# Performance work log

Hardware: AMD Instinct MI355X
Metric: run time of the kernel (lower is better)

Reference implementation:

```python
import jax, jax.numpy as jnp
import numpy as np

NUM_LAYERS = 2
HIDDEN = 512
INPUT = 512


def _lstm_cell(x, h, c, Wih, Whh, bih, bbh):
    # PyTorch LSTMCell: gates ordered i, f, g, o
    g = x @ Wih.T + bih + h @ Whh.T + bbh  # [B, 4H]
    i, f, gg, o = jnp.split(g, 4, axis=-1)
    c_new = jax.nn.sigmoid(f) * c + jax.nn.sigmoid(i) * jnp.tanh(gg)
    h_new = jax.nn.sigmoid(o) * jnp.tanh(c_new)
    return h_new, c_new


def setup_inputs() -> dict:
    key = jax.random.key(0)
    ks = jax.random.split(key, 8)
    B, T = 64, 512
    s = 1.0 / np.sqrt(HIDDEN)
    return {
        "x": jax.random.normal(ks[0], (B, T, INPUT), dtype=jnp.float32),
        "h0": jax.random.normal(ks[1], (NUM_LAYERS, B, HIDDEN), dtype=jnp.float32),
        "c0": jax.random.normal(ks[2], (NUM_LAYERS, B, HIDDEN), dtype=jnp.float32),
        # stacked per-layer weights (input_size == hidden_size so shapes match)
        "W_ih": jax.random.uniform(ks[3], (NUM_LAYERS, 4 * HIDDEN, INPUT), jnp.float32, -s, s),
        "W_hh": jax.random.uniform(ks[4], (NUM_LAYERS, 4 * HIDDEN, HIDDEN), jnp.float32, -s, s),
        "b_ih": jax.random.uniform(ks[5], (NUM_LAYERS, 4 * HIDDEN), jnp.float32, -s, s),
        "b_hh": jax.random.uniform(ks[6], (NUM_LAYERS, 4 * HIDDEN), jnp.float32, -s, s),
    }


def reference(x, h0, c0, W_ih, W_hh, b_ih, b_hh):
    # x: [B, T, D]; h0/c0: [L, B, H]
    xs = jnp.swapaxes(x, 0, 1)  # [T, B, D] for scan over time

    def step(carry, x_t):
        h, c = carry  # each [L, B, H]
        h_list, c_list = [], []
        inp = x_t
        for j in range(NUM_LAYERS):  # small static unroll over layers
            h_j, c_j = _lstm_cell(inp, h[j], c[j], W_ih[j], W_hh[j], b_ih[j], b_hh[j])
            h_list.append(h_j)
            c_list.append(c_j)
            inp = h_j
        h_new = jnp.stack(h_list, axis=0)
        c_new = jnp.stack(c_list, axis=0)
        return (h_new, c_new), inp  # output of top layer

    (h_fin, c_fin), outs = jax.lax.scan(step, (h0, c0), xs)
    out = jnp.swapaxes(outs, 0, 1)  # [B, T, H]
    return out, h_fin, c_fin
```

## Files before the change

### kernel.cpp

```cpp
#include <hip/hip_runtime.h>
#include <hip/hip_bf16.h>


#define TT 512

using short8 = __attribute__((ext_vector_type(8))) short;
using f32x4  = __attribute__((ext_vector_type(4))) float;

__device__ __forceinline__ short f2bf(float f) {
  unsigned u = __float_as_uint(f);
  u = (u + 0x7fffu + ((u >> 16) & 1u)) >> 16;
  return (short)u;
}
__device__ __forceinline__ float bf2f(short s) {
  return __uint_as_float(((unsigned)(unsigned short)s) << 16);
}
__device__ __forceinline__ float sigf(float x) { return 1.f / (1.f + __expf(-x)); }
__device__ __forceinline__ float tanh_(float x) { return 1.f - 2.f / (__expf(2.f * x) + 1.f); }

__device__ __forceinline__ void ld8_nw(short8* d,
    const short* p0, const short* p1, const short* p2, const short* p3,
    const short* p4, const short* p5, const short* p6, const short* p7) {
  asm volatile(
      "global_load_dwordx4 %0, %8, off sc0 sc1\n\t"
      "global_load_dwordx4 %1, %9, off sc0 sc1\n\t"
      "global_load_dwordx4 %2, %10, off sc0 sc1\n\t"
      "global_load_dwordx4 %3, %11, off sc0 sc1\n\t"
      "global_load_dwordx4 %4, %12, off sc0 sc1\n\t"
      "global_load_dwordx4 %5, %13, off sc0 sc1\n\t"
      "global_load_dwordx4 %6, %14, off sc0 sc1\n\t"
      "global_load_dwordx4 %7, %15, off sc0 sc1"
      : "=&v"(d[0]), "=&v"(d[1]), "=&v"(d[2]), "=&v"(d[3]),
        "=&v"(d[4]), "=&v"(d[5]), "=&v"(d[6]), "=&v"(d[7])
      : "v"(p0), "v"(p1), "v"(p2), "v"(p3),
        "v"(p4), "v"(p5), "v"(p6), "v"(p7)
      : "memory");
}

#define TIE8(A, CNT)                                                        \
  asm volatile(CNT : "+v"(A[0]), "+v"(A[1]), "+v"(A[2]), "+v"(A[3]),        \
                     "+v"(A[4]), "+v"(A[5]), "+v"(A[6]), "+v"(A[7])         \
               ::"memory")

__device__ __forceinline__ void stc_short(short* p, short v) {
  asm volatile("global_store_short %0, %1, off sc0 sc1"
               :: "v"(p), "v"((int)v) : "memory");
}
__device__ __forceinline__ void stc_int(int* p, int v) {
  asm volatile("global_store_dword %0, %1, off sc0 sc1"
               :: "v"(p), "v"(v) : "memory");
}

__device__ __forceinline__ void pollwait(const int* f0p, const int* f1p,
                                         int t0, int t1, int tid) {
  if (tid < 64) {
    int f0, f1;
    for (;;) {
      asm volatile(
          "global_load_dword %0, %2, off sc0 sc1\n\t"
          "global_load_dword %1, %3, off sc0 sc1\n\t"
          "s_waitcnt vmcnt(0)"
          : "=&v"(f0), "=&v"(f1)
          : "v"(f0p), "v"(f1p)
          : "memory");
      if (__all(f0 >= t0 && f1 >= t1)) break;
      __builtin_amdgcn_s_sleep(1);
    }
  }
  __syncthreads();
}

__global__ __launch_bounds__(256) void conv_x(const float* __restrict__ x,
                                              short* __restrict__ xo) {
  size_t g = (size_t)blockIdx.x * 256 + threadIdx.x;
  size_t i = g * 8;
  float4 v0 = *(const float4*)(x + i);
  float4 v1 = *(const float4*)(x + i + 4);
  short8 r;
  r[0] = f2bf(v0.x); r[1] = f2bf(v0.y); r[2] = f2bf(v0.z); r[3] = f2bf(v0.w);
  r[4] = f2bf(v1.x); r[5] = f2bf(v1.y); r[6] = f2bf(v1.z); r[7] = f2bf(v1.w);
  *(short8*)(xo + (i >> 9) * 1024 + (i & 511)) = r;
}

__global__ __launch_bounds__(256) void conv_w(const float* __restrict__ Wih,
                                              const float* __restrict__ Whh,
                                              short* __restrict__ wp) {
  int g = blockIdx.x * 256 + threadIdx.x;
  int l = g / 393216;
  int rem = g % 393216;
  int j8 = rem / 6144;
  int q8 = rem % 6144;
  int s, hl, bt, c, lane;
  if (q8 < 2048) {
    s = 0; hl = 0;
    int seg = q8 >> 6; bt = seg >> 4; c = seg & 15; lane = q8 & 63;
  } else {
    int q = q8 - 2048;
    s = 1;
    int seg = q >> 6; bt = seg >> 5; c = (seg >> 1) & 15; hl = seg & 1;
    lane = q & 63;
  }
  int r = lane & 15;
  int gg = r >> 2, jj = r & 3;
  int R = gg * 512 + j8 * 8 + bt * 4 + jj;
  int k = c * 32 + (lane >> 4) * 8;
  const float* src = (s ? Whh : Wih) + ((size_t)(l * 2048 + R)) * 512 + k;
  short8 o;
#pragma unroll
  for (int e = 0; e < 8; ++e) {
    float v = src[e];
    short hi = f2bf(v);
    o[e] = hl ? f2bf(v - bf2f(hi)) : hi;
  }
  *(short8*)(wp + (size_t)g * 8) = o;
}

__global__ __launch_bounds__(256) void init_state(const float* __restrict__ h0,
                                                  short* __restrict__ h0hi,
                                                  short* __restrict__ h0lo,
                                                  short* __restrict__ h1hi,
                                                  short* __restrict__ h1lo,
                                                  int* __restrict__ flags) {
  int i = blockIdx.x * 256 + threadIdx.x;
  int l = i >> 15, bj = i & 32767;
  int b = bj >> 9, j = bj & 511;
  float h = h0[i];
  short hi = f2bf(h);
  int o = (j >> 3) * 512 + b * 8 + (j & 7);
  if (l == 0) {
    h0hi[3 * 32768 + o] = hi;
    h0lo[3 * 32768 + o] = f2bf(h - bf2f(hi));
  } else {
    h1hi[1 * 32768 + o] = hi;
    h1lo[1 * 32768 + o] = f2bf(h - bf2f(hi));
  }
  if (blockIdx.x == 0 && threadIdx.x < 128) flags[threadIdx.x] = 0;
}

__global__ __launch_bounds__(512, 1) void lstm_persist(
    const short* __restrict__ wp, const float* __restrict__ c0,
    const float* __restrict__ bih, const float* __restrict__ bhh,
    short* __restrict__ h0hi, short* __restrict__ h0lo,
    short* __restrict__ h1hi, short* __restrict__ h1lo,
    int* __restrict__ flags, float* __restrict__ out) {
  extern __shared__ char smem[];
  short* lw = (short*)smem;
  float* sG = (float*)(smem + 98304);

  const int tid = threadIdx.x;
  const int layer = blockIdx.x >> 6;
  const int j8 = blockIdx.x & 63;
  const int wv = tid >> 6;
  const int kq = wv & 3;
  const int ah = wv >> 2;
  const int lane = tid & 63;
  const int m = lane & 15;
  const int koq = lane >> 4;
  const int cbase = kq << 2;

  {
    const short* src = wp + (size_t)(layer * 64 + j8) * 49152;
    for (int i = tid; i < 6144; i += 512)
      *(short8*)(lw + i * 8) = *(const short8*)(src + i * 8);
  }

  const int sb = tid >> 3, sj = tid & 7;
  const int j = (j8 << 3) + sj;
  float creg = c0[layer * 32768 + sb * 512 + j];
  float hf = 0.f;
  float bsum[4];
#pragma unroll
  for (int g = 0; g < 4; ++g)
    bsum[g] = bih[layer * 2048 + g * 512 + j] + bhh[layer * 2048 + g * 512 + j];
  __syncthreads();

  const int br0 = ((ah * 2 + 0) << 4) + m;
  const int br1 = ((ah * 2 + 1) << 4) + m;
  const short* xo = (const short*)out;
  const int* f0p = flags + lane;
  const int* f1p = flags + 64 + lane;

  f32x4 acc[2][2];

#define ZACC()                                                   \
  {                                                              \
    _Pragma("unroll") for (int u = 0; u < 2; ++u)                \
        _Pragma("unroll") for (int v = 0; v < 2; ++v)            \
            acc[u][v] = f32x4{0.f, 0.f, 0.f, 0.f};               \
  }

#define PA(rX, cc, br) \
  ((rX) + ((((cbase + (cc)) << 2) + koq) << 9) + (br) * 8)

#define HH_MFMA(Ah, Al)                                                        \
  _Pragma("unroll") for (int cc = 0; cc < 4; ++cc) {                           \
    const int c = cbase + cc;                                                  \
    short8 bh0 = *(const short8*)(lw + 16384 + (c * 2 + 0) * 512 + lane * 8);  \
    short8 bl0 = *(const short8*)(lw + 16384 + (c * 2 + 1) * 512 + lane * 8);  \
    short8 bh1 = *(const short8*)(lw + 16384 + ((16 + c) * 2 + 0) * 512 + lane * 8); \
    short8 bl1 = *(const short8*)(lw + 16384 + ((16 + c) * 2 + 1) * 512 + lane * 8); \
    _Pragma("unroll") for (int it = 0; it < 2; ++it) {                         \
      short8 a = Ah[cc * 2 + it];                                              \
      short8 al = Al[cc * 2 + it];                                             \
      acc[0][it] = __builtin_amdgcn_mfma_f32_16x16x32_bf16(a, bh0, acc[0][it], 0, 0, 0); \
      acc[0][it] = __builtin_amdgcn_mfma_f32_16x16x32_bf16(a, bl0, acc[0][it], 0, 0, 0); \
      acc[0][it] = __builtin_amdgcn_mfma_f32_16x16x32_bf16(al, bh0, acc[0][it], 0, 0, 0); \
      acc[1][it] = __builtin_amdgcn_mfma_f32_16x16x32_bf16(a, bh1, acc[1][it], 0, 0, 0); \
      acc[1][it] = __builtin_amdgcn_mfma_f32_16x16x32_bf16(a, bl1, acc[1][it], 0, 0, 0); \
      acc[1][it] = __builtin_amdgcn_mfma_f32_16x16x32_bf16(al, bh1, acc[1][it], 0, 0, 0); \
    }                                                                          \
  }

#define EPILOGUE(CN, HN)                                                       \
  _Pragma("unroll") for (int bt = 0; bt < 2; ++bt)                             \
      _Pragma("unroll") for (int it = 0; it < 2; ++it) {                       \
    const int srow = bt * 16 + m;                                              \
    const int col = ((ah * 2 + it) << 4) + (koq << 2);                         \
    _Pragma("unroll") for (int r = 0; r < 4; ++r)                              \
        sG[(kq * 32 + srow) * 66 + col + r] = acc[bt][it][r];                  \
  }                                                                            \
  __syncthreads();                                                             \
  float CN, HN;                                                                \
  {                                                                            \
    const int bt = sj >> 2, jl = sj & 3;                                       \
    float gv[4];                                                               \
    _Pragma("unroll") for (int g = 0; g < 4; ++g) {                            \
      const int s = bt * 16 + g * 4 + jl;                                      \
      gv[g] = sG[(0 * 32 + s) * 66 + sb] + sG[(1 * 32 + s) * 66 + sb] +        \
              sG[(2 * 32 + s) * 66 + sb] + sG[(3 * 32 + s) * 66 + sb] +        \
              bsum[g];                                                         \
    }                                                                          \
    CN = sigf(gv[1]) * creg + sigf(gv[0]) * tanh_(gv[2]);                      \
    HN = sigf(gv[3]) * tanh_(CN);                                              \
  }

  if (layer == 0) {
    ZACC();
#pragma unroll
    for (int cc = 0; cc < 4; ++cc) {
      const int c = cbase + cc;
      const int k = c * 32 + (koq << 3);
      short8 b0 = *(const short8*)(lw + c * 512 + lane * 8);
      short8 b1 = *(const short8*)(lw + (16 + c) * 512 + lane * 8);
#pragma unroll
      for (int it = 0; it < 2; ++it) {
        const int br = it ? br1 : br0;
        short8 a = *(const short8*)(xo + ((size_t)br * TT + 0) * 1024 + k);
        acc[0][it] = __builtin_amdgcn_mfma_f32_16x16x32_bf16(a, b0, acc[0][it], 0, 0, 0);
        acc[1][it] = __builtin_amdgcn_mfma_f32_16x16x32_bf16(a, b1, acc[1][it], 0, 0, 0);
      }
    }

    for (int p = 0; p < TT; ++p) {
      pollwait(f0p, f1p, p, p - 3, tid);

      short8 Ah[8], Al[8];
      const short* rh = h0hi + ((p - 1) & 3) * 32768;
      const short* rl = h0lo + ((p - 1) & 3) * 32768;
      ld8_nw(Ah, PA(rh, 0, br0), PA(rh, 0, br1), PA(rh, 1, br0), PA(rh, 1, br1),
                 PA(rh, 2, br0), PA(rh, 2, br1), PA(rh, 3, br0), PA(rh, 3, br1));
      ld8_nw(Al, PA(rl, 0, br0), PA(rl, 0, br1), PA(rl, 1, br0), PA(rl, 1, br1),
                 PA(rl, 2, br0), PA(rl, 2, br1), PA(rl, 3, br0), PA(rl, 3, br1));
      TIE8(Ah, "s_waitcnt vmcnt(0)");
      TIE8(Al, "");
      HH_MFMA(Ah, Al);

      EPILOGUE(cn, hn);
      creg = cn;
      hf = hn;
      {
        short* dh = h0hi + (p & 3) * 32768 + (j8 << 9) + tid;
        short* dl = h0lo + (p & 3) * 32768 + (j8 << 9) + tid;
        const short hb = f2bf(hn);
        stc_short(dh, hb);
        stc_short(dl, f2bf(hn - bf2f(hb)));
      }
      __syncthreads();
      if (tid == 0) stc_int(flags + j8, p + 1);

      if (p + 1 < TT) {
        ZACC();
#pragma unroll
        for (int cc = 0; cc < 4; ++cc) {
          const int c = cbase + cc;
          const int k = c * 32 + (koq << 3);
          short8 b0 = *(const short8*)(lw + c * 512 + lane * 8);
          short8 b1 = *(const short8*)(lw + (16 + c) * 512 + lane * 8);
#pragma unroll
          for (int it = 0; it < 2; ++it) {
            const int br = it ? br1 : br0;
            short8 a = *(const short8*)(xo + ((size_t)br * TT + p + 1) * 1024 + k);
            acc[0][it] = __builtin_amdgcn_mfma_f32_16x16x32_bf16(a, b0, acc[0][it], 0, 0, 0);
            acc[1][it] = __builtin_amdgcn_mfma_f32_16x16x32_bf16(a, b1, acc[1][it], 0, 0, 0);
          }
        }
      }
    }
  } else {
    for (int tau = 1; tau <= TT; ++tau) {
      const int tl = tau - 1;
      pollwait(f0p, f1p, tau, tau - 1, tid);

      ZACC();
      short8 Ax[8], Ah[8], Al[8];
      const short* ph = h0hi + (tl & 3) * 32768;
      const short* rh = h1hi + (tau & 1) * 32768;
      const short* rl = h1lo + (tau & 1) * 32768;
      ld8_nw(Ax, PA(ph, 0, br0), PA(ph, 0, br1), PA(ph, 1, br0), PA(ph, 1, br1),
                 PA(ph, 2, br0), PA(ph, 2, br1), PA(ph, 3, br0), PA(ph, 3, br1));
      ld8_nw(Ah, PA(rh, 0, br0), PA(rh, 0, br1), PA(rh, 1, br0), PA(rh, 1, br1),
                 PA(rh, 2, br0), PA(rh, 2, br1), PA(rh, 3, br0), PA(rh, 3, br1));
      ld8_nw(Al, PA(rl, 0, br0), PA(rl, 0, br1), PA(rl, 1, br0), PA(rl, 1, br1),
                 PA(rl, 2, br0), PA(rl, 2, br1), PA(rl, 3, br0), PA(rl, 3, br1));
      TIE8(Ax, "s_waitcnt vmcnt(16)");
#pragma unroll
      for (int cc = 0; cc < 4; ++cc) {
        const int c = cbase + cc;
        short8 b0 = *(const short8*)(lw + c * 512 + lane * 8);
        short8 b1 = *(const short8*)(lw + (16 + c) * 512 + lane * 8);
#pragma unroll
        for (int it = 0; it < 2; ++it) {
          short8 a = Ax[cc * 2 + it];
          acc[0][it] = __builtin_amdgcn_mfma_f32_16x16x32_bf16(a, b0, acc[0][it], 0, 0, 0);
          acc[1][it] = __builtin_amdgcn_mfma_f32_16x16x32_bf16(a, b1, acc[1][it], 0, 0, 0);
        }
      }
      TIE8(Ah, "s_waitcnt vmcnt(0)");
      TIE8(Al, "");
      HH_MFMA(Ah, Al);

      EPILOGUE(cn, hn);
      creg = cn;
      hf = hn;
      {
        short* dh = h1hi + ((tau + 1) & 1) * 32768 + (j8 << 9) + tid;
        short* dl = h1lo + ((tau + 1) & 1) * 32768 + (j8 << 9) + tid;
        const short hb = f2bf(hn);
        stc_short(dh, hb);
        stc_short(dl, f2bf(hn - bf2f(hb)));
      }
      __syncthreads();
      if (tid == 0) stc_int(flags + 64 + j8, tau);
      __builtin_nontemporal_store(hn, &out[((size_t)sb * 512 + tl) * 512 + j]);
    }
  }

  out[16777216 + layer * 32768 + sb * 512 + j] = hf;
  out[16777216 + 65536 + layer * 32768 + sb * 512 + j] = creg;
}


extern "C" void kernel_launch(void* const* d_in, const int* in_sizes, int n_in,
                              void* d_out, int out_size, void* d_ws,
                              size_t ws_size, hipStream_t stream) {
  const float* x = (const float*)d_in[0];
  const float* h0 = (const float*)d_in[1];
  const float* c0 = (const float*)d_in[2];
  const float* Wih = (const float*)d_in[3];
  const float* Whh = (const float*)d_in[4];
  const float* bih = (const float*)d_in[5];
  const float* bhh = (const float*)d_in[6];
  float* out = (float*)d_out;

  char* ws = (char*)d_ws;
  short* wp   = (short*)(ws + 0);
  short* h0hi = (short*)(ws + 12582912);
  short* h0lo = (short*)(ws + 12845056);
  short* h1hi = (short*)(ws + 13107200);
  short* h1lo = (short*)(ws + 13238272);
  int*  flags = (int*)(ws + 13369344);

  hipFuncSetAttribute(reinterpret_cast<const void*>(lstm_persist),
                      hipFuncAttributeMaxDynamicSharedMemorySize, 132096);

  conv_x<<<8192, 256, 0, stream>>>(x, (short*)out);
  conv_w<<<3072, 256, 0, stream>>>(Wih, Whh, wp);
  init_state<<<256, 256, 0, stream>>>(h0, h0hi, h0lo, h1hi, h1lo, flags);

  void* args[] = {(void*)&wp,   (void*)&c0,   (void*)&bih,  (void*)&bhh,
                  (void*)&h0hi, (void*)&h0lo, (void*)&h1hi, (void*)&h1lo,
                  (void*)&flags, (void*)&out};
  hipLaunchCooperativeKernel(reinterpret_cast<void*>(lstm_persist), dim3(128),
                             dim3(512), args, 132096, stream);
}
```

Measured before the change: 3.071 ms.

## Pad sync flags per cache line and split layer-1 wait into staged polls

Flags are spaced 32 ints apart so each block's flag sits on its own 128-byte line, removing false sharing during cross-block polling. Layer 1 now waits on layer-0 progress only when needed, using a cached minimum of observed layer-0 flags, and issues its layer-0 h loads before polling for layer-1 peers, overlapping load latency with the wait. An explicit vmcnt drain before the barrier makes the h stores complete before the flag is published. The cost is an extra LDS slot, an extra barrier in layer 1, and added store-drain latency on the critical path.

```diff
diff --git a/kernel.cpp b/kernel.cpp
--- a/kernel.cpp
+++ b/kernel.cpp
@@ -50,24 +50,23 @@
   asm volatile("global_store_dword %0, %1, off sc0 sc1"
                :: "v"(p), "v"(v) : "memory");
 }
-
-__device__ __forceinline__ void pollwait(const int* f0p, const int* f1p,
-                                         int t0, int t1, int tid) {
-  if (tid < 64) {
-    int f0, f1;
-    for (;;) {
-      asm volatile(
-          "global_load_dword %0, %2, off sc0 sc1\n\t"
-          "global_load_dword %1, %3, off sc0 sc1\n\t"
-          "s_waitcnt vmcnt(0)"
-          : "=&v"(f0), "=&v"(f1)
-          : "v"(f0p), "v"(f1p)
-          : "memory");
-      if (__all(f0 >= t0 && f1 >= t1)) break;
-      __builtin_amdgcn_s_sleep(1);
-    }
-  }
-  __syncthreads();
+__device__ __forceinline__ void drain_vm() {
+  asm volatile("s_waitcnt vmcnt(0)" ::: "memory");
+}
+
+__device__ __forceinline__ void pollld(int& a, int& b, const int* pa,
+                                       const int* pb) {
+  asm volatile(
+      "global_load_dword %0, %2, off sc0 sc1\n\t"
+      "global_load_dword %1, %3, off sc0 sc1\n\t"
+      "s_waitcnt vmcnt(0)"
+      : "=&v"(a), "=&v"(b) : "v"(pa), "v"(pb) : "memory");
+}
+
+__device__ __forceinline__ int wave_min(int v) {
+#pragma unroll
+  for (int o = 32; o; o >>= 1) v = min(v, __shfl_xor(v, o, 64));
+  return v;
 }
 
 __global__ __launch_bounds__(256) void conv_x(const float* __restrict__ x,
@@ -134,7 +133,7 @@
     h1hi[1 * 32768 + o] = hi;
     h1lo[1 * 32768 + o] = f2bf(h - bf2f(hi));
   }
-  if (blockIdx.x == 0 && threadIdx.x < 128) flags[threadIdx.x] = 0;
+  if (blockIdx.x == 0 && threadIdx.x < 128) flags[threadIdx.x * 32] = 0;
 }
 
 __global__ __launch_bounds__(512, 1) void lstm_persist(
@@ -146,6 +145,7 @@
   extern __shared__ char smem[];
   short* lw = (short*)smem;
   float* sG = (float*)(smem + 98304);
+  int* sf0 = (int*)(smem + 132096);
 
   const int tid = threadIdx.x;
   const int layer = blockIdx.x >> 6;
@@ -177,8 +177,8 @@
   const int br0 = ((ah * 2 + 0) << 4) + m;
   const int br1 = ((ah * 2 + 1) << 4) + m;
   const short* xo = (const short*)out;
-  const int* f0p = flags + lane;
-  const int* f1p = flags + 64 + lane;
+  const int* f0p = flags + lane * 32;
+  const int* f1p = flags + (64 + lane) * 32;
 
   f32x4 acc[2][2];
 
@@ -252,7 +252,15 @@
     }
 
     for (int p = 0; p < TT; ++p) {
-      pollwait(f0p, f1p, p, p - 3, tid);
+      if (tid < 64) {
+        int f0, f1;
+        for (;;) {
+          pollld(f0, f1, f0p, f1p);
+          if (__all(f0 >= p && f1 >= p - 3)) break;
+          __builtin_amdgcn_s_sleep(1);
+        }
+      }
+      __syncthreads();
 
       short8 Ah[8], Al[8];
       const short* rh = h0hi + ((p - 1) & 3) * 32768;
@@ -275,8 +283,9 @@
         stc_short(dh, hb);
         stc_short(dl, f2bf(hn - bf2f(hb)));
       }
+      drain_vm();
       __syncthreads();
-      if (tid == 0) stc_int(flags + j8, p + 1);
+      if (tid == 0) stc_int(flags + j8 * 32, p + 1);
 
       if (p + 1 < TT) {
         ZACC();
@@ -297,17 +306,45 @@
       }
     }
   } else {
+    int f0seen = 0;
     for (int tau = 1; tau <= TT; ++tau) {
       const int tl = tau - 1;
-      pollwait(f0p, f1p, tau, tau - 1, tid);
+
+      if (f0seen < tau) {
+        if (tid < 64) {
+          int f0, fx;
+          for (;;) {
+            pollld(f0, fx, f0p, f0p);
+            if (__all(f0 >= tau)) break;
+            __builtin_amdgcn_s_sleep(1);
+          }
+        }
+        __syncthreads();
+        f0seen = tau;
+      }
 
       ZACC();
       short8 Ax[8], Ah[8], Al[8];
       const short* ph = h0hi + (tl & 3) * 32768;
+      ld8_nw(Ax, PA(ph, 0, br0), PA(ph, 0, br1), PA(ph, 1, br0), PA(ph, 1, br1),
+                 PA(ph, 2, br0), PA(ph, 2, br1), PA(ph, 3, br0), PA(ph, 3, br1));
+
+      if (tid < 64) {
+        int f1, f0;
+        for (;;) {
+          pollld(f1, f0, f1p, f0p);
+          if (__all(f1 >= tau - 1)) break;
+          __builtin_amdgcn_s_sleep(1);
+        }
+        if (lane == 0) {}
+        int mn = wave_min(f0);
+        if (lane == 0) *sf0 = mn;
+      }
+      __syncthreads();
+      f0seen = *sf0;
+
       const short* rh = h1hi + (tau & 1) * 32768;
       const short* rl = h1lo + (tau & 1) * 32768;
-      ld8_nw(Ax, PA(ph, 0, br0), PA(ph, 0, br1), PA(ph, 1, br0), PA(ph, 1, br1),
-                 PA(ph, 2, br0), PA(ph, 2, br1), PA(ph, 3, br0), PA(ph, 3, br1));
       ld8_nw(Ah, PA(rh, 0, br0), PA(rh, 0, br1), PA(rh, 1, br0), PA(rh, 1, br1),
                  PA(rh, 2, br0), PA(rh, 2, br1), PA(rh, 3, br0), PA(rh, 3, br1));
       ld8_nw(Al, PA(rl, 0, br0), PA(rl, 0, br1), PA(rl, 1, br0), PA(rl, 1, br1),
@@ -339,8 +376,9 @@
         stc_short(dh, hb);
         stc_short(dl, f2bf(hn - bf2f(hb)));
       }
+      drain_vm();
       __syncthreads();
-      if (tid == 0) stc_int(flags + 64 + j8, tau);
+      if (tid == 0) stc_int(flags + (64 + j8) * 32, tau);
       __builtin_nontemporal_store(hn, &out[((size_t)sb * 512 + tl) * 512 + j]);
     }
   }
@@ -371,7 +409,7 @@
   int*  flags = (int*)(ws + 13369344);
 
   hipFuncSetAttribute(reinterpret_cast<const void*>(lstm_persist),
-                      hipFuncAttributeMaxDynamicSharedMemorySize, 132096);
+                      hipFuncAttributeMaxDynamicSharedMemorySize, 132352);
 
   conv_x<<<8192, 256, 0, stream>>>(x, (short*)out);
   conv_w<<<3072, 256, 0, stream>>>(Wih, Whh, wp);
@@ -381,5 +419,5 @@
                   (void*)&h0hi, (void*)&h0lo, (void*)&h1hi, (void*)&h1lo,
                   (void*)&flags, (void*)&out};
   hipLaunchCooperativeKernel(reinterpret_cast<void*>(lstm_persist), dim3(128),
-                             dim3(512), args, 132096, stream);
-}
+                             dim3(512), args, 132352, stream);
+}
```

New measurement: 2.785 ms. 1.1x faster.
